# Kernel tuning notes

Hardware: AMD Instinct MI355X
Metric: run time of the kernel (lower is better)

Reference implementation:

```python
import jax, jax.numpy as jnp
import jax.scipy.linalg as jsp
import numpy as np

# Problem dimensions (match init_kwargs P_shape/A_shape)
N = 256   # variables
M = 512   # constraints
B = 64    # batch

# OSQP ADMM hyper-parameters (fixed-rho variant of the OSQP algorithm)
SIGMA = 1e-6
RHO = 0.1
ALPHA = 1.6
N_ITERS = 500


def setup_inputs() -> dict:
    key = jax.random.key(0)
    kP, kq, kA, kc = jax.random.split(key, 4)
    # P is diagonal with strictly positive entries -> PSD (values are the nnz of P)
    P_val = jax.random.uniform(kP, (B, N), dtype=jnp.float32) + 0.1
    q_val = jax.random.normal(kq, (B, N), dtype=jnp.float32)
    # A is a dense pattern; values stored row-major as its nnz vector
    A_val = jax.random.normal(kA, (B, M * N), dtype=jnp.float32) / np.sqrt(N)
    # Feasible box: l <= u by construction
    center = jax.random.normal(kc, (B, M), dtype=jnp.float32)
    l_val = center - 1.0
    u_val = center + 1.0
    return {"P_val": P_val, "q_val": q_val, "A_val": A_val, "l_val": l_val, "u_val": u_val}


def _admm_qp(P_val, q_val, A_val, l_val, u_val):
    """Batched OSQP-style ADMM solve of min 1/2 x'Px + q'x  s.t. l <= Ax <= u.

    P is diagonal (nnz pattern = diag), A is dense (nnz pattern = full m x n).
    """
    A = A_val.reshape(B, M, N)                      # [B,m,n]
    # KKT-like matrix M_k = P + sigma*I + rho*A'A   [B,n,n]
    eye = jnp.eye(N, dtype=P_val.dtype)
    P_diag = P_val + SIGMA                          # diagonal of P + sigma*I
    Mk = RHO * jnp.einsum('bmi,bmj->bij', A, A) + jax.vmap(jnp.diag)(P_diag)
    L = jnp.linalg.cholesky(Mk)                     # [B,n,n], factor once, reuse
    Lt = jnp.swapaxes(L, -1, -2)

    def kkt_solve(rhs):                             # rhs [B,n]
        y1 = jsp.solve_triangular(L, rhs[..., None], lower=True)
        y2 = jsp.solve_triangular(Lt, y1, lower=False)
        return y2[..., 0]

    x0 = jnp.zeros((B, N), dtype=P_val.dtype)
    z0 = jnp.zeros((B, M), dtype=P_val.dtype)
    y0 = jnp.zeros((B, M), dtype=P_val.dtype)

    def step(state, _):
        x, z, y = state
        rhs = SIGMA * x - q_val + jnp.einsum('bmn,bm->bn', A, RHO * z - y)
        x_t = kkt_solve(rhs)                        # x-tilde
        z_t = jnp.einsum('bmn,bn->bm', A, x_t)      # z-tilde = A x_t
        x_new = ALPHA * x_t + (1.0 - ALPHA) * x
        z_hat = ALPHA * z_t + (1.0 - ALPHA) * z
        z_new = jnp.clip(z_hat + y / RHO, l_val, u_val)
        y_new = y + RHO * (z_hat - z_new)
        return (x_new, z_new, y_new), None

    (x, _, _), _ = jax.lax.scan(step, (x0, z0, y0), None, length=N_ITERS)
    return x


def reference(P_val, q_val, A_val, l_val, u_val):
    return _admm_qp(P_val, q_val, A_val, l_val, u_val)   # [B, n] primal solutions
```

## Files before the change

### kernel.cpp

```cpp
#include <hip/hip_runtime.h>
#include <hip/hip_fp16.h>

#define N_VAR 256
#define M_CON 512
#define BATCH 64
#define SIGMA_C 1e-6f
#define RHO_C 0.1f
#define ALPHA_C 1.6f
#define NITERS 500

__global__ __launch_bounds__(256) void k_transpose(const float* __restrict__ A,
                                                   float* __restrict__ At) {
  __shared__ float tile[32][33];
  int b = blockIdx.z;
  int n0 = blockIdx.x * 32;
  int m0 = blockIdx.y * 32;
  const float* Ab = A + (size_t)b * (M_CON * N_VAR);
  float* Atb = At + (size_t)b * (M_CON * N_VAR);
  int tx = threadIdx.x, ty = threadIdx.y;
#pragma unroll
  for (int j = 0; j < 32; j += 8)
    tile[ty + j][tx] = Ab[(size_t)(m0 + ty + j) * N_VAR + n0 + tx];
  __syncthreads();
#pragma unroll
  for (int j = 0; j < 32; j += 8)
    Atb[(size_t)(n0 + ty + j) * M_CON + m0 + tx] = tile[tx][ty + j];
}

__global__ __launch_bounds__(256) void k_ntgemm(
    const float* __restrict__ X, const float* __restrict__ Y,
    float* __restrict__ C, int I, int J, int K,
    long long bsX, long long bsY, long long bsC, float alpha,
    const float* __restrict__ diagv, int tilesJ) {
  int b = blockIdx.y;
  int ti = blockIdx.x / tilesJ, tj = blockIdx.x % tilesJ;
  int i0 = ti * 128, j0 = tj * 128;
  const float* Xb = X + (size_t)b * bsX;
  const float* Yb = Y + (size_t)b * bsY;
  float* Cb = C + (size_t)b * bsC;
  __shared__ float Xs[16][128];
  __shared__ float Ys[16][128];
  int tid = threadIdx.x;
  int tx = tid & 15, ty = tid >> 4;
  float acc[8][8];
#pragma unroll
  for (int r = 0; r < 8; ++r)
#pragma unroll
    for (int c = 0; c < 8; ++c) acc[r][c] = 0.0f;

  for (int kk = 0; kk < K; kk += 16) {
#pragma unroll
    for (int v = 0; v < 2; ++v) {
      int idx = v * 256 + tid;
      int row = idx >> 2;
      int k4 = (idx & 3) * 4;
      float4 gx = *(const float4*)(Xb + (size_t)(i0 + row) * K + kk + k4);
      Xs[k4 + 0][row] = gx.x; Xs[k4 + 1][row] = gx.y;
      Xs[k4 + 2][row] = gx.z; Xs[k4 + 3][row] = gx.w;
      float4 gy = *(const float4*)(Yb + (size_t)(j0 + row) * K + kk + k4);
      Ys[k4 + 0][row] = gy.x; Ys[k4 + 1][row] = gy.y;
      Ys[k4 + 2][row] = gy.z; Ys[k4 + 3][row] = gy.w;
    }
    __syncthreads();
#pragma unroll
    for (int k = 0; k < 16; ++k) {
      float xr[8], yr[8];
      *(float4*)&xr[0] = *(float4*)&Xs[k][ty * 8];
      *(float4*)&xr[4] = *(float4*)&Xs[k][ty * 8 + 4];
      *(float4*)&yr[0] = *(float4*)&Ys[k][tx * 8];
      *(float4*)&yr[4] = *(float4*)&Ys[k][tx * 8 + 4];
#pragma unroll
      for (int r = 0; r < 8; ++r)
#pragma unroll
        for (int c = 0; c < 8; ++c) acc[r][c] += xr[r] * yr[c];
    }
    __syncthreads();
  }
#pragma unroll
  for (int r = 0; r < 8; ++r) {
    int gi = i0 + ty * 8 + r;
#pragma unroll
    for (int c = 0; c < 8; ++c) {
      int gj = j0 + tx * 8 + c;
      float val = acc[r][c] * alpha;
      if (diagv != nullptr && gi == gj) val += diagv[(size_t)b * N_VAR + gi] + SIGMA_C;
      Cb[(size_t)gi * J + gj] = val;
    }
  }
}

__global__ __launch_bounds__(512, 2) void k_invert(const float* __restrict__ Mk,
                                                   float* __restrict__ Mi) {
  int b = blockIdx.x;
  const float* src = Mk + (size_t)b * 65536;
  float* dst = Mi + (size_t)b * 65536;
  int t = threadIdx.x;
  int c = t & 255, rh = t >> 8;

  float a[128];
#pragma unroll
  for (int j = 0; j < 128; ++j) a[j] = src[(size_t)(rh * 128 + j) * 256 + c];

  __shared__ float colPan[256][8];
  __shared__ float rowPan[2][8][260];
  __shared__ float PiSh[64];
  __shared__ float Rp[8][260];

  int rh_s = __builtin_amdgcn_readfirstlane(rh);
  int cw_s = __builtin_amdgcn_readfirstlane((t >> 6) & 3);

  if (rh == 0) {
#pragma unroll
    for (int j = 0; j < 8; ++j) rowPan[0][j][c] = a[j];
  }
  __syncthreads();

  for (int s = 0; s < 32; ++s) {
    int kb = s * 8;
    int cur = s & 1, nxt = cur ^ 1;
    int kh = kb >> 7, kj = kb & 127;
    int khn = (kb + 8) >> 7, kjn = (kb + 8) & 127;
    bool mycol = (c >= kb) && (c < kb + 8);

    if (cw_s == (kb >> 6)) {
      if (mycol) {
        int f = c - kb;
#pragma unroll
        for (int j = 0; j < 128; ++j) colPan[rh * 128 + j][f] = a[j];
      }
    }
    if (t < 64) {
      int e = t >> 3, f = t & 7;
      float p = rowPan[cur][e][kb + f];
#pragma unroll
      for (int k2 = 0; k2 < 8; ++k2) {
        float piv = __shfl(p, k2 * 8 + k2);
        float rv = __shfl(p, k2 * 8 + f);
        float cv = __shfl(p, e * 8 + k2);
        float pivinv = 1.0f / piv;
        float srv = rv * pivinv;
        float gen = p - cv * srv;
        p = gen;
        if (e == k2) p = srv;
        if (f == k2) p = -cv * pivinv;
        if (e == k2 && f == k2) p = pivinv;
      }
      PiSh[t] = p;
    }
    __syncthreads();

    float rpan[8];
#pragma unroll
    for (int f2 = 0; f2 < 8; ++f2) rpan[f2] = rowPan[cur][f2][c];
    float rp[8];
#pragma unroll
    for (int e = 0; e < 8; ++e) {
      float4 p0 = *(const float4*)&PiSh[e * 8];
      float4 p1 = *(const float4*)&PiSh[e * 8 + 4];
      rp[e] = p0.x * rpan[0] + p0.y * rpan[1] + p0.z * rpan[2] + p0.w * rpan[3] +
              p1.x * rpan[4] + p1.y * rpan[5] + p1.z * rpan[6] + p1.w * rpan[7];
    }
    if (cw_s == (kb >> 6)) {
      if (mycol) {
        int f = c - kb;
#pragma unroll
        for (int e = 0; e < 8; ++e) rp[e] = PiSh[e * 8 + f];
      }
    }
#pragma unroll
    for (int e = 0; e < 8; ++e) Rp[e][c] = rp[e];

    bool myhalfk = (rh_s == kh);
    bool stashw = (s != 31) && (rh_s == khn);
#pragma unroll
    for (int j = 0; j < 128; ++j) {
      float4 c0 = *(const float4*)&colPan[rh * 128 + j][0];
      float4 c1 = *(const float4*)&colPan[rh * 128 + j][4];
      float aold = a[j];
      float nv = aold -
                 (c0.x * rp[0] + c0.y * rp[1] + c0.z * rp[2] + c0.w * rp[3] +
                  c1.x * rp[4] + c1.y * rp[5] + c1.z * rp[6] + c1.w * rp[7]);
      if (mycol) nv -= aold;
      if (myhalfk && j >= kj && j < kj + 8)
        nv = Rp[j - kj][c];
      a[j] = nv;
      if (stashw && j >= kjn && j < kjn + 8)
        rowPan[nxt][j - kjn][c] = nv;
    }
    __syncthreads();
  }

#pragma unroll
  for (int j = 0; j < 128; ++j) dst[(size_t)(rh * 128 + j) * 256 + c] = a[j];
}

__global__ __launch_bounds__(256) void k_matvec_h(const float* __restrict__ Mi,
                                                  const float* __restrict__ q,
                                                  float* __restrict__ h) {
  int b = blockIdx.x, t = threadIdx.x;
  __shared__ float qs[256];
  qs[t] = q[(size_t)b * 256 + t];
  __syncthreads();
  const float* Mb = Mi + (size_t)b * 65536;
  float acc = 0.0f;
  for (int k = 0; k < 256; ++k) acc += Mb[(size_t)k * 256 + t] * qs[k];
  h[(size_t)b * 256 + t] = acc;
}

__global__ __launch_bounds__(512) void k_matvec_d(const float* __restrict__ At,
                                                  const float* __restrict__ h,
                                                  float* __restrict__ d) {
  int b = blockIdx.x, t = threadIdx.x;
  __shared__ float hs[256];
  if (t < 256) hs[t] = h[(size_t)b * 256 + t];
  __syncthreads();
  const float* Ab = At + (size_t)b * 131072;
  float acc = 0.0f;
  for (int n = 0; n < 256; ++n) acc += Ab[(size_t)n * 512 + t] * hs[n];
  d[(size_t)b * 512 + t] = acc;
}

__global__ __launch_bounds__(512) void k_admm4(
    const float* __restrict__ G, const float* __restrict__ dvec,
    const float* __restrict__ lv, const float* __restrict__ uv,
    unsigned long long* __restrict__ wtag, float* __restrict__ Sbuf) {
  int g = blockIdx.x;
  int b = (g & 7) + 8 * ((g >> 3) & 7);
  int s = g >> 6;
  int t = threadIdx.x;
  int l = t & 63, wv = t >> 6;
  int c0 = wv * 64;

  __shared__ __align__(16) float wbuf[8][64];
  __shared__ float part[2][8][128];

  const float* Gb = G + (size_t)b * 262144;
  const float* g0p = Gb + (size_t)(s * 128 + l) * 512 + c0;
  const float* g1p = Gb + (size_t)(s * 128 + 64 + l) * 512 + c0;
  float G0[64], G1[64];
#pragma unroll
  for (int j = 0; j < 16; ++j) {
    float4 v0 = *(const float4*)(g0p + 4 * j);
    G0[4 * j + 0] = v0.x; G0[4 * j + 1] = v0.y;
    G0[4 * j + 2] = v0.z; G0[4 * j + 3] = v0.w;
    float4 v1 = *(const float4*)(g1p + 4 * j);
    G1[4 * j + 0] = v1.x; G1[4 * j + 1] = v1.y;
    G1[4 * j + 2] = v1.z; G1[4 * j + 3] = v1.w;
  }
#pragma unroll
  for (int j = 0; j < 64; ++j) {
    asm volatile("" : "+v"(G0[j]));
    asm volatile("" : "+v"(G1[j]));
  }

  float zreg = 0.0f, yreg = 0.0f, Sreg = 0.0f;
  float lreg = 0.0f, ureg = 0.0f, dreg = 0.0f;
  if (t < 128) {
    lreg = lv[(size_t)b * 512 + s * 128 + t];
    ureg = uv[(size_t)b * 512 + s * 128 + t];
    dreg = dvec[(size_t)b * 512 + s * 128 + t];
  }
  wbuf[wv][l] = 0.0f;

  unsigned long long* wt0 = wtag + (size_t)b * 512;
  unsigned long long* wt1 = wtag + 32768 + (size_t)b * 512;
  const float4* wq4 = (const float4*)(wbuf[wv]);

  for (int it = 0; it < NITERS; ++it) {
    if (it > 0) {
      unsigned long long* wp = (it & 1) ? wt1 : wt0;
      unsigned want = (unsigned)it;
      unsigned long long v = __hip_atomic_load(&wp[c0 + l], __ATOMIC_RELAXED,
                                               __HIP_MEMORY_SCOPE_AGENT);
      bool got = ((unsigned)(v >> 32) == want);
      while (!__all(got)) {
        if (!got) {
          unsigned long long v2 = __hip_atomic_load(
              &wp[c0 + l], __ATOMIC_RELAXED, __HIP_MEMORY_SCOPE_AGENT);
          if ((unsigned)(v2 >> 32) == want) { v = v2; got = true; }
        }
      }
      wbuf[wv][l] = __uint_as_float((unsigned)(v & 0xffffffffu));
    }

    float r0a = 0.f, r0b = 0.f, r1a = 0.f, r1b = 0.f;
#pragma unroll
    for (int j = 0; j < 8; ++j) {
      float4 wa = wq4[2 * j];
      float4 wc = wq4[2 * j + 1];
      r0a += G0[8 * j + 0] * wa.x + G0[8 * j + 1] * wa.y +
             G0[8 * j + 2] * wa.z + G0[8 * j + 3] * wa.w;
      r1a += G1[8 * j + 0] * wa.x + G1[8 * j + 1] * wa.y +
             G1[8 * j + 2] * wa.z + G1[8 * j + 3] * wa.w;
      r0b += G0[8 * j + 4] * wc.x + G0[8 * j + 5] * wc.y +
             G0[8 * j + 6] * wc.z + G0[8 * j + 7] * wc.w;
      r1b += G1[8 * j + 4] * wc.x + G1[8 * j + 5] * wc.y +
             G1[8 * j + 6] * wc.z + G1[8 * j + 7] * wc.w;
    }
    int pp = it & 1;
    part[pp][wv][l] = r0a + r0b;
    part[pp][wv][64 + l] = r1a + r1b;
    __syncthreads();

    if (t < 128) {
      float w_old = RHO_C * zreg - yreg;
      Sreg = w_old - 0.6f * Sreg;
      float p = part[pp][0][t] + part[pp][1][t] + part[pp][2][t] +
                part[pp][3][t] + part[pp][4][t] + part[pp][5][t] +
                part[pp][6][t] + part[pp][7][t];
      float zt = p - dreg;
      float zh = ALPHA_C * zt + (1.0f - ALPHA_C) * zreg;
      float zc = zh + yreg * (1.0f / RHO_C);
      zc = fminf(fmaxf(zc, lreg), ureg);
      yreg += RHO_C * (zh - zc);
      zreg = zc;
      if (it < NITERS - 1) {
        float wn = RHO_C * zreg - yreg;
        unsigned long long pk =
            ((unsigned long long)(unsigned)(it + 1) << 32) |
            (unsigned long long)__float_as_uint(wn);
        unsigned long long* wp = ((it + 1) & 1) ? wt1 : wt0;
        __hip_atomic_store(&wp[s * 128 + t], pk, __ATOMIC_RELAXED,
                           __HIP_MEMORY_SCOPE_AGENT);
      }
    }
  }

  if (t < 128) Sbuf[(size_t)b * 512 + s * 128 + t] = Sreg;
}

__global__ __launch_bounds__(256) void k_final(
    const float* __restrict__ A, const float* __restrict__ q,
    const float* __restrict__ Mi, const float* __restrict__ Sbuf,
    float* __restrict__ xout) {
  int b = blockIdx.x, t = threadIdx.x;
  __shared__ float Ssh[512];
  __shared__ float uu[256];
  for (int i = t; i < 512; i += 256) Ssh[i] = Sbuf[(size_t)b * 512 + i];
  __syncthreads();
  const float* Ab = A + (size_t)b * 131072;
  float acc = 0.0f;
  for (int m = 0; m < 512; ++m) acc += Ab[(size_t)m * 256 + t] * Ssh[m];
  uu[t] = ALPHA_C * acc - q[(size_t)b * 256 + t];
  __syncthreads();
  const float* Mb = Mi + (size_t)b * 65536;
  float x = 0.0f;
  for (int kk = 0; kk < 256; ++kk) x += Mb[(size_t)kk * 256 + t] * uu[kk];
  xout[(size_t)b * 256 + t] = x;
}

extern "C" void kernel_launch(void* const* d_in, const int* in_sizes, int n_in,
                              void* d_out, int out_size, void* d_ws, size_t ws_size,
                              hipStream_t stream) {
  (void)in_sizes; (void)n_in; (void)out_size; (void)ws_size;
  const float* P = (const float*)d_in[0];
  const float* q = (const float*)d_in[1];
  const float* Av = (const float*)d_in[2];
  const float* lv = (const float*)d_in[3];
  const float* uv = (const float*)d_in[4];
  float* xout = (float*)d_out;

  float* ws = (float*)d_ws;
  float* At = ws;
  float* F  = ws;
  float* Mi = ws + 8388608;
  float* Mk = ws + 12582912;
  float* G  = ws + 12582912;
  float* hv = ws + 29360128;
  float* dv = ws + 29376512;
  float* Sbuf = ws + 29409280;
  unsigned long long* wtag = (unsigned long long*)ws;

  k_transpose<<<dim3(8, 16, 64), dim3(32, 8), 0, stream>>>(Av, At);
  k_ntgemm<<<dim3(4, 64), 256, 0, stream>>>(At, At, Mk, 256, 256, 512,
                                            131072LL, 131072LL, 65536LL,
                                            RHO_C, P, 2);
  k_invert<<<64, 512, 0, stream>>>(Mk, Mi);
  k_matvec_h<<<64, 256, 0, stream>>>(Mi, q, hv);
  k_matvec_d<<<64, 512, 0, stream>>>(At, hv, dv);
  k_ntgemm<<<dim3(8, 64), 256, 0, stream>>>(Av, Mi, F, 512, 256, 256,
                                            131072LL, 65536LL, 131072LL,
                                            1.0f, nullptr, 2);
  k_ntgemm<<<dim3(16, 64), 256, 0, stream>>>(F, Av, G, 512, 512, 256,
                                             131072LL, 131072LL, 262144LL,
                                             1.0f, nullptr, 4);
  k_admm4<<<256, 512, 0, stream>>>(G, dv, lv, uv, wtag, Sbuf);
  k_final<<<64, 256, 0, stream>>>(Av, q, Mi, Sbuf, xout);
}
```

Baseline: 1.615 ms.

## Store G in packed fp16 in shared memory and restructure ADMM matvec partition

The G = A Mi A' GEMM now writes its output as packed half2 values in a layout tailored to the ADMM kernel. The ADMM kernel keeps most of that half-precision G block in LDS and a small remainder in registers, instead of holding 128 fp32 values per thread in registers. Each wave now handles 128 columns for one 64-row half, which cuts the partial-sum reduction from 8 terms to 4. The spin-wait adds s_sleep. This lowers register pressure and memory traffic but adds fp16 rounding to G, which can change accuracy over 500 iterations, and moves the matvec reads to LDS.

```diff
diff --git a/kernel.cpp b/kernel.cpp
--- a/kernel.cpp
+++ b/kernel.cpp
@@ -31,7 +31,7 @@
     const float* __restrict__ X, const float* __restrict__ Y,
     float* __restrict__ C, int I, int J, int K,
     long long bsX, long long bsY, long long bsC, float alpha,
-    const float* __restrict__ diagv, int tilesJ) {
+    const float* __restrict__ diagv, int tilesJ, int packC) {
   int b = blockIdx.y;
   int ti = blockIdx.x / tilesJ, tj = blockIdx.x % tilesJ;
   int i0 = ti * 128, j0 = tj * 128;
@@ -75,6 +75,24 @@
         for (int c = 0; c < 8; ++c) acc[r][c] += xr[r] * yr[c];
     }
     __syncthreads();
+  }
+  if (packC) {
+    unsigned* Cp = (unsigned*)Cb;
+#pragma unroll
+    for (int r = 0; r < 8; ++r) {
+      int gi = i0 + ty * 8 + r;
+      int sl = gi >> 7, rl = gi & 127;
+      int rh = rl >> 6, ll = rl & 63;
+#pragma unroll
+      for (int c = 0; c < 8; c += 2) {
+        int gj = j0 + tx * 8 + c;
+        int cg = gj >> 7, j2 = (gj & 127) >> 1;
+        int t2 = ((((cg << 1) | rh) << 6) | ll);
+        __half2 hh = __floats2half2_rn(acc[r][c] * alpha, acc[r][c + 1] * alpha);
+        Cp[(size_t)sl * 32768 + j2 * 512 + t2] = *(unsigned*)&hh;
+      }
+    }
+    return;
   }
 #pragma unroll
   for (int r = 0; r < 8; ++r) {
@@ -221,7 +239,7 @@
 }
 
 __global__ __launch_bounds__(512) void k_admm4(
-    const float* __restrict__ G, const float* __restrict__ dvec,
+    const unsigned* __restrict__ Gpk_g, const float* __restrict__ dvec,
     const float* __restrict__ lv, const float* __restrict__ uv,
     unsigned long long* __restrict__ wtag, float* __restrict__ Sbuf) {
   int g = blockIdx.x;
@@ -229,29 +247,22 @@
   int s = g >> 6;
   int t = threadIdx.x;
   int l = t & 63, wv = t >> 6;
-  int c0 = wv * 64;
-
-  __shared__ __align__(16) float wbuf[8][64];
-  __shared__ float part[2][8][128];
-
-  const float* Gb = G + (size_t)b * 262144;
-  const float* g0p = Gb + (size_t)(s * 128 + l) * 512 + c0;
-  const float* g1p = Gb + (size_t)(s * 128 + 64 + l) * 512 + c0;
-  float G0[64], G1[64];
-#pragma unroll
-  for (int j = 0; j < 16; ++j) {
-    float4 v0 = *(const float4*)(g0p + 4 * j);
-    G0[4 * j + 0] = v0.x; G0[4 * j + 1] = v0.y;
-    G0[4 * j + 2] = v0.z; G0[4 * j + 3] = v0.w;
-    float4 v1 = *(const float4*)(g1p + 4 * j);
-    G1[4 * j + 0] = v1.x; G1[4 * j + 1] = v1.y;
-    G1[4 * j + 2] = v1.z; G1[4 * j + 3] = v1.w;
-  }
-#pragma unroll
-  for (int j = 0; j < 64; ++j) {
-    asm volatile("" : "+v"(G0[j]));
-    asm volatile("" : "+v"(G1[j]));
-  }
+  int rh = wv & 1, cg = wv >> 1;
+  int c0 = cg * 128;
+  int row_local = rh * 64 + l;
+
+  __shared__ unsigned Gpk[56][512];
+  __shared__ __align__(16) float wbufp[8][128];
+  __shared__ float part[2][4][128];
+
+  const unsigned* gsrc = Gpk_g + (size_t)(b * 4 + s) * 32768;
+#pragma unroll
+  for (int j2 = 0; j2 < 56; ++j2) Gpk[j2][t] = gsrc[j2 * 512 + t];
+  unsigned gq[8];
+#pragma unroll
+  for (int j2 = 0; j2 < 8; ++j2) gq[j2] = gsrc[(56 + j2) * 512 + t];
+#pragma unroll
+  for (int j2 = 0; j2 < 8; ++j2) asm volatile("" : "+v"(gq[j2]));
 
   float zreg = 0.0f, yreg = 0.0f, Sreg = 0.0f;
   float lreg = 0.0f, ureg = 0.0f, dreg = 0.0f;
@@ -260,54 +271,66 @@
     ureg = uv[(size_t)b * 512 + s * 128 + t];
     dreg = dvec[(size_t)b * 512 + s * 128 + t];
   }
-  wbuf[wv][l] = 0.0f;
+  wbufp[wv][l] = 0.0f;
+  wbufp[wv][64 + l] = 0.0f;
 
   unsigned long long* wt0 = wtag + (size_t)b * 512;
   unsigned long long* wt1 = wtag + 32768 + (size_t)b * 512;
-  const float4* wq4 = (const float4*)(wbuf[wv]);
+  const float* wrow = wbufp[wv];
 
   for (int it = 0; it < NITERS; ++it) {
     if (it > 0) {
       unsigned long long* wp = (it & 1) ? wt1 : wt0;
       unsigned want = (unsigned)it;
-      unsigned long long v = __hip_atomic_load(&wp[c0 + l], __ATOMIC_RELAXED,
-                                               __HIP_MEMORY_SCOPE_AGENT);
-      bool got = ((unsigned)(v >> 32) == want);
-      while (!__all(got)) {
-        if (!got) {
-          unsigned long long v2 = __hip_atomic_load(
+      unsigned long long v0 = __hip_atomic_load(&wp[c0 + l], __ATOMIC_RELAXED,
+                                                __HIP_MEMORY_SCOPE_AGENT);
+      unsigned long long v1 = __hip_atomic_load(&wp[c0 + 64 + l], __ATOMIC_RELAXED,
+                                                __HIP_MEMORY_SCOPE_AGENT);
+      bool g0 = ((unsigned)(v0 >> 32) == want);
+      bool g1 = ((unsigned)(v1 >> 32) == want);
+      while (!__all(g0 && g1)) {
+        __builtin_amdgcn_s_sleep(1);
+        if (!g0) {
+          unsigned long long x = __hip_atomic_load(
               &wp[c0 + l], __ATOMIC_RELAXED, __HIP_MEMORY_SCOPE_AGENT);
-          if ((unsigned)(v2 >> 32) == want) { v = v2; got = true; }
+          if ((unsigned)(x >> 32) == want) { v0 = x; g0 = true; }
         }
-      }
-      wbuf[wv][l] = __uint_as_float((unsigned)(v & 0xffffffffu));
-    }
-
-    float r0a = 0.f, r0b = 0.f, r1a = 0.f, r1b = 0.f;
-#pragma unroll
-    for (int j = 0; j < 8; ++j) {
-      float4 wa = wq4[2 * j];
-      float4 wc = wq4[2 * j + 1];
-      r0a += G0[8 * j + 0] * wa.x + G0[8 * j + 1] * wa.y +
-             G0[8 * j + 2] * wa.z + G0[8 * j + 3] * wa.w;
-      r1a += G1[8 * j + 0] * wa.x + G1[8 * j + 1] * wa.y +
-             G1[8 * j + 2] * wa.z + G1[8 * j + 3] * wa.w;
-      r0b += G0[8 * j + 4] * wc.x + G0[8 * j + 5] * wc.y +
-             G0[8 * j + 6] * wc.z + G0[8 * j + 7] * wc.w;
-      r1b += G1[8 * j + 4] * wc.x + G1[8 * j + 5] * wc.y +
-             G1[8 * j + 6] * wc.z + G1[8 * j + 7] * wc.w;
+        if (!g1) {
+          unsigned long long x = __hip_atomic_load(
+              &wp[c0 + 64 + l], __ATOMIC_RELAXED, __HIP_MEMORY_SCOPE_AGENT);
+          if ((unsigned)(x >> 32) == want) { v1 = x; g1 = true; }
+        }
+      }
+      wbufp[wv][l] = __uint_as_float((unsigned)(v0 & 0xffffffffu));
+      wbufp[wv][64 + l] = __uint_as_float((unsigned)(v1 & 0xffffffffu));
+    }
+
+    float acc = 0.0f;
+#pragma unroll
+    for (int j2 = 0; j2 < 56; j2 += 2) {
+      float4 wq = *(const float4*)&wrow[j2 * 2];
+      unsigned ga = Gpk[j2][t];
+      unsigned gb = Gpk[j2 + 1][t];
+      float2 fa = __half22float2(*(__half2*)&ga);
+      float2 fb = __half22float2(*(__half2*)&gb);
+      acc += fa.x * wq.x + fa.y * wq.y + fb.x * wq.z + fb.y * wq.w;
+    }
+#pragma unroll
+    for (int j2 = 56; j2 < 64; j2 += 2) {
+      float4 wq = *(const float4*)&wrow[j2 * 2];
+      float2 fa = __half22float2(*(__half2*)&gq[j2 - 56]);
+      float2 fb = __half22float2(*(__half2*)&gq[j2 - 55]);
+      acc += fa.x * wq.x + fa.y * wq.y + fb.x * wq.z + fb.y * wq.w;
     }
     int pp = it & 1;
-    part[pp][wv][l] = r0a + r0b;
-    part[pp][wv][64 + l] = r1a + r1b;
+    part[pp][cg][row_local] = acc;
     __syncthreads();
 
     if (t < 128) {
       float w_old = RHO_C * zreg - yreg;
       Sreg = w_old - 0.6f * Sreg;
       float p = part[pp][0][t] + part[pp][1][t] + part[pp][2][t] +
-                part[pp][3][t] + part[pp][4][t] + part[pp][5][t] +
-                part[pp][6][t] + part[pp][7][t];
+                part[pp][3][t];
       float zt = p - dreg;
       float zh = ALPHA_C * zt + (1.0f - ALPHA_C) * zreg;
       float zc = zh + yreg * (1.0f / RHO_C);
@@ -365,7 +388,7 @@
   float* F  = ws;
   float* Mi = ws + 8388608;
   float* Mk = ws + 12582912;
-  float* G  = ws + 12582912;
+  float* Gp = ws + 12582912;
   float* hv = ws + 29360128;
   float* dv = ws + 29376512;
   float* Sbuf = ws + 29409280;
@@ -374,16 +397,16 @@
   k_transpose<<<dim3(8, 16, 64), dim3(32, 8), 0, stream>>>(Av, At);
   k_ntgemm<<<dim3(4, 64), 256, 0, stream>>>(At, At, Mk, 256, 256, 512,
                                             131072LL, 131072LL, 65536LL,
-                                            RHO_C, P, 2);
+                                            RHO_C, P, 2, 0);
   k_invert<<<64, 512, 0, stream>>>(Mk, Mi);
   k_matvec_h<<<64, 256, 0, stream>>>(Mi, q, hv);
   k_matvec_d<<<64, 512, 0, stream>>>(At, hv, dv);
   k_ntgemm<<<dim3(8, 64), 256, 0, stream>>>(Av, Mi, F, 512, 256, 256,
                                             131072LL, 65536LL, 131072LL,
-                                            1.0f, nullptr, 2);
-  k_ntgemm<<<dim3(16, 64), 256, 0, stream>>>(F, Av, G, 512, 512, 256,
-                                             131072LL, 131072LL, 262144LL,
-                                             1.0f, nullptr, 4);
-  k_admm4<<<256, 512, 0, stream>>>(G, dv, lv, uv, wtag, Sbuf);
+                                            1.0f, nullptr, 2, 0);
+  k_ntgemm<<<dim3(16, 64), 256, 0, stream>>>(F, Av, Gp, 512, 512, 256,
+                                             131072LL, 131072LL, 131072LL,
+                                             1.0f, nullptr, 4, 1);
+  k_admm4<<<256, 512, 0, stream>>>((const unsigned*)Gp, dv, lv, uv, wtag, Sbuf);
   k_final<<<64, 256, 0, stream>>>(Av, q, Mi, Sbuf, xout);
 }
```

Measured after the change: 2.070 ms. 28.2% more time.

## Store G as packed fp16 and stream it from memory in ADMM loop

Applied to the files above, without the earlier changes.

The G-producing GEMM now writes G = A·Mi·Aᵀ as packed half2 in a layout matched to the ADMM kernel's access pattern. The ADMM kernel no longer holds its 128 G values per thread in registers; it reloads the halves from global memory or cache each iteration and converts them to float. This halves G's footprint and frees many VGPRs, but adds memory traffic on every one of the 500 iterations and loses precision in G.

```diff
diff --git a/kernel.cpp b/kernel.cpp
--- a/kernel.cpp
+++ b/kernel.cpp
@@ -31,7 +31,7 @@
     const float* __restrict__ X, const float* __restrict__ Y,
     float* __restrict__ C, int I, int J, int K,
     long long bsX, long long bsY, long long bsC, float alpha,
-    const float* __restrict__ diagv, int tilesJ) {
+    const float* __restrict__ diagv, int tilesJ, int packC) {
   int b = blockIdx.y;
   int ti = blockIdx.x / tilesJ, tj = blockIdx.x % tilesJ;
   int i0 = ti * 128, j0 = tj * 128;
@@ -75,6 +75,24 @@
         for (int c = 0; c < 8; ++c) acc[r][c] += xr[r] * yr[c];
     }
     __syncthreads();
+  }
+  if (packC) {
+    unsigned* Cp = (unsigned*)Cb;
+#pragma unroll
+    for (int r = 0; r < 8; ++r) {
+      int gi = i0 + ty * 8 + r;
+      int sl = gi >> 7, rl = gi & 127;
+      int rh = rl >> 6, ll = rl & 63;
+#pragma unroll
+      for (int c = 0; c < 8; c += 2) {
+        int gj = j0 + tx * 8 + c;
+        int cg = gj >> 7, j2 = (gj & 127) >> 1;
+        int t2 = ((((cg << 1) | rh) << 6) | ll);
+        __half2 hh = __floats2half2_rn(acc[r][c] * alpha, acc[r][c + 1] * alpha);
+        Cp[(size_t)sl * 32768 + j2 * 512 + t2] = *(unsigned*)&hh;
+      }
+    }
+    return;
   }
 #pragma unroll
   for (int r = 0; r < 8; ++r) {
@@ -221,7 +239,7 @@
 }
 
 __global__ __launch_bounds__(512) void k_admm4(
-    const float* __restrict__ G, const float* __restrict__ dvec,
+    const unsigned* __restrict__ Gpk_g, const float* __restrict__ dvec,
     const float* __restrict__ lv, const float* __restrict__ uv,
     unsigned long long* __restrict__ wtag, float* __restrict__ Sbuf) {
   int g = blockIdx.x;
@@ -230,28 +248,13 @@
   int t = threadIdx.x;
   int l = t & 63, wv = t >> 6;
   int c0 = wv * 64;
+  int cg = wv >> 1, hc = wv & 1;
 
   __shared__ __align__(16) float wbuf[8][64];
   __shared__ float part[2][8][128];
 
-  const float* Gb = G + (size_t)b * 262144;
-  const float* g0p = Gb + (size_t)(s * 128 + l) * 512 + c0;
-  const float* g1p = Gb + (size_t)(s * 128 + 64 + l) * 512 + c0;
-  float G0[64], G1[64];
-#pragma unroll
-  for (int j = 0; j < 16; ++j) {
-    float4 v0 = *(const float4*)(g0p + 4 * j);
-    G0[4 * j + 0] = v0.x; G0[4 * j + 1] = v0.y;
-    G0[4 * j + 2] = v0.z; G0[4 * j + 3] = v0.w;
-    float4 v1 = *(const float4*)(g1p + 4 * j);
-    G1[4 * j + 0] = v1.x; G1[4 * j + 1] = v1.y;
-    G1[4 * j + 2] = v1.z; G1[4 * j + 3] = v1.w;
-  }
-#pragma unroll
-  for (int j = 0; j < 64; ++j) {
-    asm volatile("" : "+v"(G0[j]));
-    asm volatile("" : "+v"(G1[j]));
-  }
+  const unsigned* gsrc =
+      Gpk_g + (size_t)(b * 4 + s) * 32768 + (size_t)(hc * 32) * 512 + cg * 128 + l;
 
   float zreg = 0.0f, yreg = 0.0f, Sreg = 0.0f;
   float lreg = 0.0f, ureg = 0.0f, dreg = 0.0f;
@@ -288,14 +291,26 @@
     for (int j = 0; j < 8; ++j) {
       float4 wa = wq4[2 * j];
       float4 wc = wq4[2 * j + 1];
-      r0a += G0[8 * j + 0] * wa.x + G0[8 * j + 1] * wa.y +
-             G0[8 * j + 2] * wa.z + G0[8 * j + 3] * wa.w;
-      r1a += G1[8 * j + 0] * wa.x + G1[8 * j + 1] * wa.y +
-             G1[8 * j + 2] * wa.z + G1[8 * j + 3] * wa.w;
-      r0b += G0[8 * j + 4] * wc.x + G0[8 * j + 5] * wc.y +
-             G0[8 * j + 6] * wc.z + G0[8 * j + 7] * wc.w;
-      r1b += G1[8 * j + 4] * wc.x + G1[8 * j + 5] * wc.y +
-             G1[8 * j + 6] * wc.z + G1[8 * j + 7] * wc.w;
+      unsigned a0 = gsrc[(4 * j + 0) * 512];
+      unsigned a1 = gsrc[(4 * j + 1) * 512];
+      unsigned a2 = gsrc[(4 * j + 2) * 512];
+      unsigned a3 = gsrc[(4 * j + 3) * 512];
+      unsigned b0 = gsrc[(4 * j + 0) * 512 + 64];
+      unsigned b1 = gsrc[(4 * j + 1) * 512 + 64];
+      unsigned b2 = gsrc[(4 * j + 2) * 512 + 64];
+      unsigned b3 = gsrc[(4 * j + 3) * 512 + 64];
+      float2 fa0 = __half22float2(*(__half2*)&a0);
+      float2 fa1 = __half22float2(*(__half2*)&a1);
+      float2 fa2 = __half22float2(*(__half2*)&a2);
+      float2 fa3 = __half22float2(*(__half2*)&a3);
+      float2 fb0 = __half22float2(*(__half2*)&b0);
+      float2 fb1 = __half22float2(*(__half2*)&b1);
+      float2 fb2 = __half22float2(*(__half2*)&b2);
+      float2 fb3 = __half22float2(*(__half2*)&b3);
+      r0a += fa0.x * wa.x + fa0.y * wa.y + fa1.x * wa.z + fa1.y * wa.w;
+      r0b += fa2.x * wc.x + fa2.y * wc.y + fa3.x * wc.z + fa3.y * wc.w;
+      r1a += fb0.x * wa.x + fb0.y * wa.y + fb1.x * wa.z + fb1.y * wa.w;
+      r1b += fb2.x * wc.x + fb2.y * wc.y + fb3.x * wc.z + fb3.y * wc.w;
     }
     int pp = it & 1;
     part[pp][wv][l] = r0a + r0b;
@@ -365,7 +380,7 @@
   float* F  = ws;
   float* Mi = ws + 8388608;
   float* Mk = ws + 12582912;
-  float* G  = ws + 12582912;
+  float* Gp = ws + 12582912;
   float* hv = ws + 29360128;
   float* dv = ws + 29376512;
   float* Sbuf = ws + 29409280;
@@ -374,16 +389,16 @@
   k_transpose<<<dim3(8, 16, 64), dim3(32, 8), 0, stream>>>(Av, At);
   k_ntgemm<<<dim3(4, 64), 256, 0, stream>>>(At, At, Mk, 256, 256, 512,
                                             131072LL, 131072LL, 65536LL,
-                                            RHO_C, P, 2);
+                                            RHO_C, P, 2, 0);
   k_invert<<<64, 512, 0, stream>>>(Mk, Mi);
   k_matvec_h<<<64, 256, 0, stream>>>(Mi, q, hv);
   k_matvec_d<<<64, 512, 0, stream>>>(At, hv, dv);
   k_ntgemm<<<dim3(8, 64), 256, 0, stream>>>(Av, Mi, F, 512, 256, 256,
                                             131072LL, 65536LL, 131072LL,
-                                            1.0f, nullptr, 2);
-  k_ntgemm<<<dim3(16, 64), 256, 0, stream>>>(F, Av, G, 512, 512, 256,
-                                             131072LL, 131072LL, 262144LL,
-                                             1.0f, nullptr, 4);
-  k_admm4<<<256, 512, 0, stream>>>(G, dv, lv, uv, wtag, Sbuf);
+                                            1.0f, nullptr, 2, 0);
+  k_ntgemm<<<dim3(16, 64), 256, 0, stream>>>(F, Av, Gp, 512, 512, 256,
+                                             131072LL, 131072LL, 131072LL,
+                                             1.0f, nullptr, 4, 1);
+  k_admm4<<<256, 512, 0, stream>>>((const unsigned*)Gp, dv, lv, uv, wtag, Sbuf);
   k_final<<<64, 256, 0, stream>>>(Av, q, Mi, Sbuf, xout);
 }
```

Result: faster. 1.541 ms (-4.5%).
